# Optimization experiments

Hardware: AMD Instinct MI355X
Metric: run time of the kernel (lower is better)

Reference implementation:

```python
import jax, jax.numpy as jnp
import numpy as np

# Config constants (match init_kwargs)
D_MODEL = 1024
D_MLP = 2048
NUM_EXPERTS = 8
EXPERTS_PER_TOKEN = 2
BATCH, SEQ = 2, 2048


def setup_inputs() -> dict:
    key = jax.random.key(0)
    k0, k1, k2, k3, k4 = jax.random.split(key, 5)
    init = lambda k, shape: jax.random.normal(k, shape, jnp.float32) * 0.02
    return {
        "x": jax.random.normal(k0, (BATCH, SEQ, D_MODEL), jnp.float32),
        "W_router": init(k1, (D_MODEL, NUM_EXPERTS)),
        "W_gate": init(k2, (NUM_EXPERTS, D_MODEL, D_MLP)),
        "W_in": init(k3, (NUM_EXPERTS, D_MODEL, D_MLP)),
        "W_out": init(k4, (NUM_EXPERTS, D_MLP, D_MODEL)),
    }


def reference(x, W_router, W_gate, W_in, W_out):
    B, S, D = x.shape
    h = x.reshape(-1, D)                                  # [T, D]
    T = h.shape[0]
    E = W_router.shape[1]

    # Router: softmax in fp32, top-k, renormalize (as in torch source)
    router_logits = h @ W_router                          # [T, E]
    probs = jax.nn.softmax(router_logits.astype(jnp.float32), axis=-1)
    top_w, top_i = jax.lax.top_k(probs, EXPERTS_PER_TOKEN)  # [T, K]
    top_w = top_w / top_w.sum(axis=-1, keepdims=True)
    top_w = top_w.astype(h.dtype)

    # Dense combine matrix [T, E]; top-k indices are distinct per token
    combine = jnp.zeros((T, E), h.dtype).at[jnp.arange(T)[:, None], top_i].set(top_w)

    # GatedMLP per expert: silu(h @ Wg) * (h @ Wi) @ Wo  (computed densely over experts,
    # then combined with the sparse routing weights -> same math as gather/MLP/scatter loop)
    gate_pre = jnp.einsum('td,edf->etf', h, W_gate)       # [E, T, F]
    up = jnp.einsum('td,edf->etf', h, W_in)               # [E, T, F]
    act = jax.nn.silu(gate_pre) * up                      # [E, T, F]
    expert_out = jnp.einsum('etf,efd->etd', act, W_out)   # [E, T, D]

    out = jnp.einsum('etd,te->td', expert_out, combine)   # [T, D]
    return out.reshape(B, S, D), router_logits
```

## Files before the change

### kernel.cpp

```cpp
#include <hip/hip_runtime.h>
#include <cstdint>
#include <cstddef>

#define T_TOK 4096
#define DM 1024
#define DF 2048
#define NE 8
#define PADROWS 9216
#define MAXTILES 72

typedef unsigned short u16;
typedef unsigned int u32;
using short8 = __attribute__((ext_vector_type(8))) short;
using f32x4  = __attribute__((ext_vector_type(4))) float;

static constexpr size_t OFF_H    = 0;
static constexpr size_t OFF_WGT  = OFF_H   + (size_t)T_TOK * DM * 2;
static constexpr size_t OFF_WIT  = OFF_WGT + (size_t)NE * DM * DF * 2;
static constexpr size_t OFF_WOT  = OFF_WIT + (size_t)NE * DM * DF * 2;
static constexpr size_t OFF_A    = OFF_WOT + (size_t)NE * DF * DM * 2;
static constexpr size_t OFF_TOK  = OFF_A   + (size_t)PADROWS * DF * 2;
static constexpr size_t OFF_WL   = OFF_TOK + PADROWS * 4;
static constexpr size_t OFF_TEXP = OFF_WL  + PADROWS * 4;
static constexpr size_t OFF_TW   = OFF_TEXP + (size_t)T_TOK * 2 * 4;
static constexpr size_t OFF_CNT  = OFF_TW  + (size_t)T_TOK * 2 * 4;
static constexpr size_t OFF_CUR  = OFF_CNT + 64;
static constexpr size_t OFF_NT   = OFF_CUR + 64;
static constexpr size_t OFF_TE   = OFF_NT  + 64;
static constexpr size_t OFF_TP   = OFF_TE  + 512;
static constexpr size_t OFF_POS  = OFF_TP  + 512;

__device__ __forceinline__ u16 f2bf(float f) {
  u32 u = __builtin_bit_cast(u32, f);
  u += 0x7FFFu + ((u >> 16) & 1u);
  return (u16)(u >> 16);
}
__device__ __forceinline__ float bf2f(u16 b) {
  u32 u = ((u32)b) << 16;
  return __builtin_bit_cast(float, u);
}

__device__ __forceinline__ void async16(const void* g, void* l) {
  __builtin_amdgcn_global_load_lds((__attribute__((address_space(1))) void*)(g),
                                   (__attribute__((address_space(3))) void*)(l),
                                   16, 0, 0);
}

__global__ void init_small_k(int* __restrict__ tok, float* __restrict__ wl,
                             int* __restrict__ cnt) {
  int i = blockIdx.x * 256 + threadIdx.x;
  if (i < PADROWS) { tok[i] = -1; wl[i] = 0.f; }
  if (i < NE) cnt[i] = 0;
}

__global__ void transpose_w_k(const float* __restrict__ Wg, const float* __restrict__ Wi,
                              const float* __restrict__ Wo, u16* __restrict__ wgT,
                              u16* __restrict__ wiT, u16* __restrict__ woT) {
  __shared__ u16 lT[64][65];
  int bid = blockIdx.x;
  int mat = bid >> 12;
  int r = bid & 4095;
  const float* src; u16* dst; int R, C;
  if (mat == 0)      { src = Wg; dst = wgT; R = DM; C = DF; }
  else if (mat == 1) { src = Wi; dst = wiT; R = DM; C = DF; }
  else               { src = Wo; dst = woT; R = DF; C = DM; }
  int e = r >> 9;
  int rem = r & 511;
  int ctiles = C >> 6;
  int tr = rem / ctiles, tc = rem % ctiles;
  size_t eb = (size_t)e * R * C;
  int r0 = tr * 64, c0 = tc * 64;
  int wv = threadIdx.x >> 6, lane = threadIdx.x & 63;
#pragma unroll
  for (int it = 0; it < 16; ++it) {
    int rl = it * 4 + wv;
    float v = src[eb + (size_t)(r0 + rl) * C + c0 + lane];
    lT[lane][rl] = f2bf(v);
  }
  __syncthreads();
#pragma unroll
  for (int i = 0; i < 2; ++i) {
    const int cl = i * 32 + wv * 8 + (lane >> 3);
    const int b8 = (lane & 7) * 8;
    u16 tmp[8];
#pragma unroll
    for (int k = 0; k < 8; ++k) tmp[k] = lT[cl][b8 + k];
    *(short8*)&dst[eb + (size_t)(c0 + cl) * R + r0 + b8] = *(const short8*)tmp;
  }
}

__global__ void router_k(const float* __restrict__ x, const float* __restrict__ Wr,
                         float* __restrict__ logits, int* __restrict__ texp,
                         float* __restrict__ tw, int* __restrict__ cnt,
                         u16* __restrict__ hbf) {
  int wv = threadIdx.x >> 6, lane = threadIdx.x & 63;
  int t = blockIdx.x * 4 + wv;
  const float* h = x + (size_t)t * DM;
  u16* hb = hbf + (size_t)t * DM;
  float acc[8] = {0.f, 0.f, 0.f, 0.f, 0.f, 0.f, 0.f, 0.f};
#pragma unroll
  for (int j = 0; j < 16; ++j) {
    float hv = h[lane + j * 64];
    hb[lane + j * 64] = f2bf(hv);
    const float4* wr = (const float4*)(Wr + (size_t)(lane + j * 64) * 8);
    float4 w0 = wr[0], w1 = wr[1];
    acc[0] += hv * w0.x; acc[1] += hv * w0.y; acc[2] += hv * w0.z; acc[3] += hv * w0.w;
    acc[4] += hv * w1.x; acc[5] += hv * w1.y; acc[6] += hv * w1.z; acc[7] += hv * w1.w;
  }
#pragma unroll
  for (int e = 0; e < 8; ++e)
#pragma unroll
    for (int off = 32; off > 0; off >>= 1) acc[e] += __shfl_down(acc[e], off, 64);
  if (lane == 0) {
    float mx = acc[0];
#pragma unroll
    for (int e = 1; e < 8; ++e) mx = fmaxf(mx, acc[e]);
    float p[8];
#pragma unroll
    for (int e = 0; e < 8; ++e) p[e] = __expf(acc[e] - mx);
    int i1 = 0; float b1 = p[0];
#pragma unroll
    for (int e = 1; e < 8; ++e) if (p[e] > b1) { b1 = p[e]; i1 = e; }
    int i2 = -1; float b2 = -1.f;
#pragma unroll
    for (int e = 0; e < 8; ++e) if (e != i1 && p[e] > b2) { b2 = p[e]; i2 = e; }
    float inv = 1.f / (b1 + b2);
    texp[t * 2] = i1; texp[t * 2 + 1] = i2;
    tw[t * 2] = b1 * inv; tw[t * 2 + 1] = b2 * inv;
    atomicAdd(&cnt[i1], 1); atomicAdd(&cnt[i2], 1);
#pragma unroll
    for (int e = 0; e < 8; ++e) logits[(size_t)t * 8 + e] = acc[e];
  }
}

__global__ void plan_k(const int* __restrict__ cnt, int* __restrict__ cursor,
                       int* __restrict__ tile_e, int* __restrict__ tile_p,
                       int* __restrict__ ntiles) {
  __shared__ int toff[NE + 1], roff[NE];
  const int l = threadIdx.x;
  if (l == 0) {
    int o = 0, nt = 0;
    for (int e = 0; e < NE; ++e) {
      int t = (cnt[e] + 127) >> 7;
      cursor[e] = o; toff[e] = nt; roff[e] = o;
      nt += t; o += t * 128;
    }
    toff[NE] = nt;
    *ntiles = nt;
  }
  __syncthreads();
  for (int idx = l; idx < MAXTILES; idx += 64) {
    int e = 0;
    while (e < NE && !(idx >= toff[e] && idx < toff[e + 1])) ++e;
    if (e < NE) { tile_e[idx] = e; tile_p[idx] = roff[e] + (idx - toff[e]) * 128; }
  }
}

__global__ void scatter_k(const int* __restrict__ texp, const float* __restrict__ tw,
                          int* __restrict__ cursor, int* __restrict__ tok,
                          float* __restrict__ wl, int* __restrict__ pos) {
  int t = blockIdx.x * 256 + threadIdx.x;
#pragma unroll
  for (int k = 0; k < 2; ++k) {
    int e = texp[t * 2 + k];
    int p = atomicAdd(&cursor[e], 1);
    tok[p] = t;
    wl[p] = tw[t * 2 + k];
    pos[t * 2 + k] = p;
  }
}

__global__ __launch_bounds__(256) void gemm1_k(
    const u16* __restrict__ hbf, const u16* __restrict__ wgT, const u16* __restrict__ wiT,
    const int* __restrict__ tok, const float* __restrict__ wl,
    const int* __restrict__ tile_e, const int* __restrict__ tile_p,
    const int* __restrict__ ntiles, u16* __restrict__ Aact) {
  __shared__ char smem[65536];
  const int tile = blockIdx.y;
  if (tile >= *ntiles) return;
  const int e  = tile_e[tile];
  const int p0 = tile_p[tile];
  const int f0 = blockIdx.x * 64;
  const int tid = threadIdx.x, wv = tid >> 6, lane = tid & 63;

  const u16* hsrc[4];
  int hoff[4];
#pragma unroll
  for (int i = 0; i < 4; ++i) {
    const int row = wv * 32 + i * 8 + (lane >> 3);
    const int gc  = (lane & 7) ^ (row & 7);
    int tk  = tok[p0 + row];
    if (tk < 0) tk = 0;
    hsrc[i] = hbf + (size_t)tk * DM + gc * 8;
    hoff[i] = (wv * 32 + i * 8) * 64;
  }
  const u16* wbase = ((wv < 2) ? wgT : wiT) + (size_t)e * DM * DF;
  const int half = wv & 1, mt = wv >> 1;
  const u16* bsrc[4];
  int boff[4];
#pragma unroll
  for (int i = 0; i < 4; ++i) {
    const int row = half * 32 + i * 8 + (lane >> 3);
    const int gc  = (lane & 7) ^ (row & 7);
    bsrc[i] = wbase + (size_t)(f0 + row) * DM + gc * 8;
    boff[i] = 8192 + mt * 4096 + (half * 32 + i * 8) * 64;
  }

  f32x4 accG[4][2], accU[4][2];
#pragma unroll
  for (int m = 0; m < 4; ++m)
#pragma unroll
    for (int n = 0; n < 2; ++n) { accG[m][n] = (f32x4)(0.f); accU[m][n] = (f32x4)(0.f); }

  const int wr = wv >> 1, wc = wv & 1;
  const int wrBase = wr * 64, wcBase = wc * 32;
  const int l4 = lane >> 4, ln = lane & 15;

  {
    u16* b = (u16*)smem;
#pragma unroll
    for (int i = 0; i < 4; ++i) async16(hsrc[i], b + hoff[i]);
#pragma unroll
    for (int i = 0; i < 4; ++i) async16(bsrc[i], b + boff[i]);
  }
  __syncthreads();

  int cur = 0;
  for (int kt = 0; kt < DM / 64; ++kt) {
    if (kt < DM / 64 - 1) {
      u16* b = (u16*)smem + (cur ^ 1) * 16384;
#pragma unroll
      for (int i = 0; i < 4; ++i) async16(hsrc[i] + (size_t)(kt + 1) * 64, b + hoff[i]);
#pragma unroll
      for (int i = 0; i < 4; ++i) async16(bsrc[i] + (size_t)(kt + 1) * 64, b + boff[i]);
    }
    const u16* b = (const u16*)smem + cur * 16384;
#pragma unroll
    for (int s = 0; s < 2; ++s) {
      const int c = s * 4 + l4;
      short8 a[4], bg[2], bu[2];
#pragma unroll
      for (int m = 0; m < 4; ++m) {
        const int row = wrBase + m * 16 + ln;
        a[m] = *(const short8*)&b[row * 64 + ((c ^ (row & 7)) * 8)];
      }
#pragma unroll
      for (int n = 0; n < 2; ++n) {
        const int rowb = wcBase + n * 16 + ln;
        const int so = rowb * 64 + ((c ^ (rowb & 7)) * 8);
        bg[n] = *(const short8*)&b[8192 + so];
        bu[n] = *(const short8*)&b[12288 + so];
      }
#pragma unroll
      for (int m = 0; m < 4; ++m)
#pragma unroll
        for (int n = 0; n < 2; ++n) {
          accG[m][n] = __builtin_amdgcn_mfma_f32_16x16x32_bf16(a[m], bg[n], accG[m][n], 0, 0, 0);
          accU[m][n] = __builtin_amdgcn_mfma_f32_16x16x32_bf16(a[m], bu[n], accU[m][n], 0, 0, 0);
        }
    }
    __syncthreads();
    cur ^= 1;
  }

  u16* lOut = (u16*)smem;
#pragma unroll
  for (int m = 0; m < 4; ++m)
#pragma unroll
    for (int j = 0; j < 4; ++j) {
      const int row = wrBase + m * 16 + l4 * 4 + j;
      const float w = wl[p0 + row];
#pragma unroll
      for (int n = 0; n < 2; ++n) {
        const float g = accG[m][n][j];
        const float u = accU[m][n][j];
        const float val = (g / (1.f + __expf(-g))) * u * w;
        lOut[row * 80 + wcBase + n * 16 + ln] = f2bf(val);
      }
    }
  __syncthreads();
  const int r = tid >> 1, hf = tid & 1;
  u16* gdst = Aact + (size_t)(p0 + r) * DF + f0 + hf * 32;
  const u16* lsrc = &lOut[r * 80 + hf * 32];
#pragma unroll
  for (int i = 0; i < 4; ++i)
    *(short8*)(gdst + i * 8) = *(const short8*)(lsrc + i * 8);
}

__global__ __launch_bounds__(256) void gemm2_k(
    const u16* __restrict__ Aact, const u16* __restrict__ woT,
    const int* __restrict__ tile_e, const int* __restrict__ tile_p,
    const int* __restrict__ ntiles, u16* __restrict__ scr) {
  __shared__ char smem[49152];
  const int tile = blockIdx.y;
  if (tile >= *ntiles) return;
  const int e  = tile_e[tile];
  const int p0 = tile_p[tile];
  const int d0 = blockIdx.x * 64;
  const int tid = threadIdx.x, wv = tid >> 6, lane = tid & 63;

  const u16* asrc[4];
  int aoff[4];
#pragma unroll
  for (int i = 0; i < 4; ++i) {
    const int row = wv * 32 + i * 8 + (lane >> 3);
    const int gc  = (lane & 7) ^ (row & 7);
    asrc[i] = Aact + (size_t)(p0 + row) * DF + gc * 8;
    aoff[i] = (wv * 32 + i * 8) * 64;
  }
  const u16* wb = woT + (size_t)e * DM * DF;
  const u16* wsrc[2];
  int woff[2];
#pragma unroll
  for (int i = 0; i < 2; ++i) {
    const int row = wv * 16 + i * 8 + (lane >> 3);
    const int gc  = (lane & 7) ^ (row & 7);
    wsrc[i] = wb + (size_t)(d0 + row) * DF + gc * 8;
    woff[i] = 8192 + (wv * 16 + i * 8) * 64;
  }

  f32x4 acc[4][2];
#pragma unroll
  for (int m = 0; m < 4; ++m)
#pragma unroll
    for (int n = 0; n < 2; ++n) acc[m][n] = (f32x4)(0.f);

  const int wr = wv >> 1, wc = wv & 1;
  const int wrBase = wr * 64, wcBase = wc * 32;
  const int l4 = lane >> 4, ln = lane & 15;

  {
    u16* b = (u16*)smem;
#pragma unroll
    for (int i = 0; i < 4; ++i) async16(asrc[i], b + aoff[i]);
#pragma unroll
    for (int i = 0; i < 2; ++i) async16(wsrc[i], b + woff[i]);
  }
  __syncthreads();

  int cur = 0;
  for (int kt = 0; kt < DF / 64; ++kt) {
    if (kt < DF / 64 - 1) {
      u16* b = (u16*)smem + (cur ^ 1) * 12288;
#pragma unroll
      for (int i = 0; i < 4; ++i) async16(asrc[i] + (size_t)(kt + 1) * 64, b + aoff[i]);
#pragma unroll
      for (int i = 0; i < 2; ++i) async16(wsrc[i] + (size_t)(kt + 1) * 64, b + woff[i]);
    }
    const u16* b = (const u16*)smem + cur * 12288;
#pragma unroll
    for (int s = 0; s < 2; ++s) {
      const int c = s * 4 + l4;
      short8 a[4], bw[2];
#pragma unroll
      for (int m = 0; m < 4; ++m) {
        const int row = wrBase + m * 16 + ln;
        a[m] = *(const short8*)&b[row * 64 + ((c ^ (row & 7)) * 8)];
      }
#pragma unroll
      for (int n = 0; n < 2; ++n) {
        const int rowb = wcBase + n * 16 + ln;
        bw[n] = *(const short8*)&b[8192 + rowb * 64 + ((c ^ (rowb & 7)) * 8)];
      }
#pragma unroll
      for (int m = 0; m < 4; ++m)
#pragma unroll
        for (int n = 0; n < 2; ++n)
          acc[m][n] = __builtin_amdgcn_mfma_f32_16x16x32_bf16(a[m], bw[n], acc[m][n], 0, 0, 0);
    }
    __syncthreads();
    cur ^= 1;
  }

  u16* lOut = (u16*)smem;
#pragma unroll
  for (int m = 0; m < 4; ++m)
#pragma unroll
    for (int j = 0; j < 4; ++j) {
      const int row = wrBase + m * 16 + l4 * 4 + j;
#pragma unroll
      for (int n = 0; n < 2; ++n)
        lOut[row * 72 + wcBase + n * 16 + ln] = f2bf(acc[m][n][j]);
    }
  __syncthreads();
  const int r = tid >> 1, hf = tid & 1;
  u16* gdst = scr + (size_t)(p0 + r) * DM + d0 + hf * 32;
  const u16* lsrc = &lOut[r * 72 + hf * 32];
#pragma unroll
  for (int i = 0; i < 4; ++i)
    *(short8*)(gdst + i * 8) = *(const short8*)(lsrc + i * 8);
}

__global__ void combine_k(const u16* __restrict__ scr, const int* __restrict__ pos,
                          float* __restrict__ out) {
  const int t = blockIdx.x;
  const int d = threadIdx.x;
  const int p1 = pos[t * 2], p2 = pos[t * 2 + 1];
  const ushort4 a = *(const ushort4*)(scr + (size_t)p1 * DM + d * 4);
  const ushort4 b = *(const ushort4*)(scr + (size_t)p2 * DM + d * 4);
  float4 o;
  o.x = bf2f(a.x) + bf2f(b.x);
  o.y = bf2f(a.y) + bf2f(b.y);
  o.z = bf2f(a.z) + bf2f(b.z);
  o.w = bf2f(a.w) + bf2f(b.w);
  *(float4*)(out + (size_t)t * DM + d * 4) = o;
}

extern "C" void kernel_launch(void* const* d_in, const int* in_sizes, int n_in,
                              void* d_out, int out_size, void* d_ws, size_t ws_size,
                              hipStream_t stream) {
  const float* x  = (const float*)d_in[0];
  const float* Wr = (const float*)d_in[1];
  const float* Wg = (const float*)d_in[2];
  const float* Wi = (const float*)d_in[3];
  const float* Wo = (const float*)d_in[4];
  float* outF = (float*)d_out;
  float* logits = outF + (size_t)T_TOK * DM;

  char* ws = (char*)d_ws;
  u16*  hbf   = (u16*)(ws + OFF_H);
  u16*  wgT   = (u16*)(ws + OFF_WGT);
  u16*  wiT   = (u16*)(ws + OFF_WIT);
  u16*  woT   = (u16*)(ws + OFF_WOT);
  u16*  Aact  = (u16*)(ws + OFF_A);
  int*  tok   = (int*)(ws + OFF_TOK);
  float* wl   = (float*)(ws + OFF_WL);
  int*  texp  = (int*)(ws + OFF_TEXP);
  float* tw   = (float*)(ws + OFF_TW);
  int*  cnt   = (int*)(ws + OFF_CNT);
  int*  cur   = (int*)(ws + OFF_CUR);
  int*  nt    = (int*)(ws + OFF_NT);
  int*  te    = (int*)(ws + OFF_TE);
  int*  tp    = (int*)(ws + OFF_TP);
  int*  pos   = (int*)(ws + OFF_POS);
  u16*  scr   = (u16*)(ws + OFF_WGT);

  init_small_k<<<40, 256, 0, stream>>>(tok, wl, cnt);
  transpose_w_k<<<12288, 256, 0, stream>>>(Wg, Wi, Wo, wgT, wiT, woT);
  router_k<<<1024, 256, 0, stream>>>(x, Wr, logits, texp, tw, cnt, hbf);
  plan_k<<<1, 64, 0, stream>>>(cnt, cur, te, tp, nt);
  scatter_k<<<16, 256, 0, stream>>>(texp, tw, cur, tok, wl, pos);
  gemm1_k<<<dim3(DF / 64, MAXTILES), 256, 0, stream>>>(hbf, wgT, wiT, tok, wl, te, tp, nt, Aact);
  gemm2_k<<<dim3(DM / 64, MAXTILES), 256, 0, stream>>>(Aact, woT, te, tp, nt, scr);
  combine_k<<<4096, 256, 0, stream>>>(scr, pos, outF);
}
```

Measured before the change: 347.1 us.

## Load GEMM weight operands directly to registers with 4-stage LDS pipeline for activations

Both expert GEMMs now read the B (weight) fragments straight from global memory into registers, double-buffered, instead of staging them through LDS. The activation tile goes through a 4-slot LDS ring with manual vmcnt waits and a single barrier per k-step, and MFMA blocks are wrapped in s_setprio. Separately, the plan and scatter kernels are merged into one single-block kernel that uses LDS atomics for the cursors. The aim is to cut LDS traffic and barrier stalls and deepen prefetch, at the cost of uncoalesced per-lane global weight loads, higher register pressure, and a serialized scatter running in one block.

```diff
diff --git a/kernel.cpp b/kernel.cpp
--- a/kernel.cpp
+++ b/kernel.cpp
@@ -45,6 +45,9 @@
                                    (__attribute__((address_space(3))) void*)(l),
                                    16, 0, 0);
 }
+
+#define VMW(N) asm volatile("s_waitcnt vmcnt(" #N ")" ::: "memory")
+#define BAR() __builtin_amdgcn_s_barrier()
 
 __global__ void init_small_k(int* __restrict__ tok, float* __restrict__ wl,
                              int* __restrict__ cnt) {
@@ -133,40 +136,38 @@
   }
 }
 
-__global__ void plan_k(const int* __restrict__ cnt, int* __restrict__ cursor,
-                       int* __restrict__ tile_e, int* __restrict__ tile_p,
-                       int* __restrict__ ntiles) {
+__global__ void plan_scatter_k(const int* __restrict__ cnt, const int* __restrict__ texp,
+                               const float* __restrict__ tw, int* __restrict__ tile_e,
+                               int* __restrict__ tile_p, int* __restrict__ ntiles,
+                               int* __restrict__ tok, float* __restrict__ wl,
+                               int* __restrict__ pos) {
+  __shared__ int curs[NE];
   __shared__ int toff[NE + 1], roff[NE];
-  const int l = threadIdx.x;
-  if (l == 0) {
-    int o = 0, nt = 0;
+  if (threadIdx.x == 0) {
+    int off = 0, nt = 0;
     for (int e = 0; e < NE; ++e) {
-      int t = (cnt[e] + 127) >> 7;
-      cursor[e] = o; toff[e] = nt; roff[e] = o;
-      nt += t; o += t * 128;
+      int tt = (cnt[e] + 127) >> 7;
+      curs[e] = off; toff[e] = nt; roff[e] = off;
+      nt += tt; off += tt * 128;
     }
     toff[NE] = nt;
     *ntiles = nt;
   }
   __syncthreads();
-  for (int idx = l; idx < MAXTILES; idx += 64) {
+  for (int idx = threadIdx.x; idx < MAXTILES; idx += 256) {
     int e = 0;
     while (e < NE && !(idx >= toff[e] && idx < toff[e + 1])) ++e;
     if (e < NE) { tile_e[idx] = e; tile_p[idx] = roff[e] + (idx - toff[e]) * 128; }
   }
-}
-
-__global__ void scatter_k(const int* __restrict__ texp, const float* __restrict__ tw,
-                          int* __restrict__ cursor, int* __restrict__ tok,
-                          float* __restrict__ wl, int* __restrict__ pos) {
-  int t = blockIdx.x * 256 + threadIdx.x;
-#pragma unroll
-  for (int k = 0; k < 2; ++k) {
-    int e = texp[t * 2 + k];
-    int p = atomicAdd(&cursor[e], 1);
-    tok[p] = t;
-    wl[p] = tw[t * 2 + k];
-    pos[t * 2 + k] = p;
+  for (int t = threadIdx.x; t < T_TOK; t += 256) {
+#pragma unroll
+    for (int k = 0; k < 2; ++k) {
+      int e = texp[t * 2 + k];
+      int p = atomicAdd(&curs[e], 1);
+      tok[p] = t;
+      wl[p] = tw[t * 2 + k];
+      pos[t * 2 + k] = p;
+    }
   }
 }
 
@@ -175,7 +176,7 @@
     const int* __restrict__ tok, const float* __restrict__ wl,
     const int* __restrict__ tile_e, const int* __restrict__ tile_p,
     const int* __restrict__ ntiles, u16* __restrict__ Aact) {
-  __shared__ char smem[65536];
+  __shared__ u16 smem[4 * 8192];
   const int tile = blockIdx.y;
   if (tile >= *ntiles) return;
   const int e  = tile_e[tile];
@@ -194,76 +195,87 @@
     hsrc[i] = hbf + (size_t)tk * DM + gc * 8;
     hoff[i] = (wv * 32 + i * 8) * 64;
   }
-  const u16* wbase = ((wv < 2) ? wgT : wiT) + (size_t)e * DM * DF;
-  const int half = wv & 1, mt = wv >> 1;
-  const u16* bsrc[4];
-  int boff[4];
-#pragma unroll
-  for (int i = 0; i < 4; ++i) {
-    const int row = half * 32 + i * 8 + (lane >> 3);
-    const int gc  = (lane & 7) ^ (row & 7);
-    bsrc[i] = wbase + (size_t)(f0 + row) * DM + gc * 8;
-    boff[i] = 8192 + mt * 4096 + (half * 32 + i * 8) * 64;
-  }
-
-  f32x4 accG[4][2], accU[4][2];
-#pragma unroll
-  for (int m = 0; m < 4; ++m)
-#pragma unroll
-    for (int n = 0; n < 2; ++n) { accG[m][n] = (f32x4)(0.f); accU[m][n] = (f32x4)(0.f); }
 
   const int wr = wv >> 1, wc = wv & 1;
   const int wrBase = wr * 64, wcBase = wc * 32;
   const int l4 = lane >> 4, ln = lane & 15;
 
-  {
-    u16* b = (u16*)smem;
-#pragma unroll
-    for (int i = 0; i < 4; ++i) async16(hsrc[i], b + hoff[i]);
-#pragma unroll
-    for (int i = 0; i < 4; ++i) async16(bsrc[i], b + boff[i]);
-  }
-  __syncthreads();
-
-  int cur = 0;
-  for (int kt = 0; kt < DM / 64; ++kt) {
-    if (kt < DM / 64 - 1) {
-      u16* b = (u16*)smem + (cur ^ 1) * 16384;
-#pragma unroll
-      for (int i = 0; i < 4; ++i) async16(hsrc[i] + (size_t)(kt + 1) * 64, b + hoff[i]);
-#pragma unroll
-      for (int i = 0; i < 4; ++i) async16(bsrc[i] + (size_t)(kt + 1) * 64, b + boff[i]);
-    }
-    const u16* b = (const u16*)smem + cur * 16384;
+  const u16* bgb[2];
+  const u16* bub[2];
+#pragma unroll
+  for (int n = 0; n < 2; ++n) {
+    const size_t rowf = (size_t)(f0 + wcBase + n * 16 + ln);
+    bgb[n] = wgT + (size_t)e * DM * DF + rowf * DM + l4 * 8;
+    bub[n] = wiT + (size_t)e * DM * DF + rowf * DM + l4 * 8;
+  }
+
+  f32x4 accG[4][2], accU[4][2];
+#pragma unroll
+  for (int m = 0; m < 4; ++m)
+#pragma unroll
+    for (int n = 0; n < 2; ++n) { accG[m][n] = (f32x4)(0.f); accU[m][n] = (f32x4)(0.f); }
+
+  short8 bg0[2][2], bu0[2][2], bg1[2][2], bu1[2][2];
+
+  auto stageH = [&](int T) {
+    u16* dst = smem + (T & 3) * 8192;
+#pragma unroll
+    for (int i = 0; i < 4; ++i) async16(hsrc[i] + (size_t)T * 64, dst + hoff[i]);
+  };
+  auto loadB = [&](short8 (&bg)[2][2], short8 (&bu)[2][2], int T) {
+#pragma unroll
+    for (int n = 0; n < 2; ++n)
+#pragma unroll
+      for (int s = 0; s < 2; ++s) {
+        bg[n][s] = *(const short8*)(bgb[n] + (size_t)T * 64 + s * 32);
+        bu[n][s] = *(const short8*)(bub[n] + (size_t)T * 64 + s * 32);
+      }
+  };
+  auto comp = [&](const short8 (&bg)[2][2], const short8 (&bu)[2][2], int slot) {
+    const u16* b = smem + slot * 8192;
+    short8 a[4][2];
 #pragma unroll
     for (int s = 0; s < 2; ++s) {
       const int c = s * 4 + l4;
-      short8 a[4], bg[2], bu[2];
 #pragma unroll
       for (int m = 0; m < 4; ++m) {
         const int row = wrBase + m * 16 + ln;
-        a[m] = *(const short8*)&b[row * 64 + ((c ^ (row & 7)) * 8)];
+        a[m][s] = *(const short8*)&b[row * 64 + ((c ^ (row & 7)) * 8)];
       }
-#pragma unroll
-      for (int n = 0; n < 2; ++n) {
-        const int rowb = wcBase + n * 16 + ln;
-        const int so = rowb * 64 + ((c ^ (rowb & 7)) * 8);
-        bg[n] = *(const short8*)&b[8192 + so];
-        bu[n] = *(const short8*)&b[12288 + so];
-      }
+    }
+    __builtin_amdgcn_s_setprio(1);
+#pragma unroll
+    for (int s = 0; s < 2; ++s)
 #pragma unroll
       for (int m = 0; m < 4; ++m)
 #pragma unroll
         for (int n = 0; n < 2; ++n) {
-          accG[m][n] = __builtin_amdgcn_mfma_f32_16x16x32_bf16(a[m], bg[n], accG[m][n], 0, 0, 0);
-          accU[m][n] = __builtin_amdgcn_mfma_f32_16x16x32_bf16(a[m], bu[n], accU[m][n], 0, 0, 0);
+          accG[m][n] = __builtin_amdgcn_mfma_f32_16x16x32_bf16(a[m][s], bg[n][s], accG[m][n], 0, 0, 0);
+          accU[m][n] = __builtin_amdgcn_mfma_f32_16x16x32_bf16(a[m][s], bu[n][s], accU[m][n], 0, 0, 0);
         }
-    }
-    __syncthreads();
-    cur ^= 1;
-  }
-
-  u16* lOut = (u16*)smem;
+    __builtin_amdgcn_s_setprio(0);
+  };
+
+  stageH(0);
+  loadB(bg0, bu0, 0);
+  stageH(1);
+  VMW(4); BAR();
+
+  for (int t = 0; t < 14; t += 2) {
+    loadB(bg1, bu1, t + 1); stageH(t + 2);
+    comp(bg0, bu0, t & 3);
+    VMW(12); BAR();
+    loadB(bg0, bu0, t + 2); stageH(t + 3);
+    comp(bg1, bu1, (t + 1) & 3);
+    VMW(12); BAR();
+  }
+  loadB(bg1, bu1, 15);
+  comp(bg0, bu0, 2);
+  VMW(8); BAR();
+  comp(bg1, bu1, 3);
+
+  u16* lOut = smem;
+  BAR();
 #pragma unroll
   for (int m = 0; m < 4; ++m)
 #pragma unroll
@@ -291,7 +303,7 @@
     const u16* __restrict__ Aact, const u16* __restrict__ woT,
     const int* __restrict__ tile_e, const int* __restrict__ tile_p,
     const int* __restrict__ ntiles, u16* __restrict__ scr) {
-  __shared__ char smem[49152];
+  __shared__ u16 smem[4 * 8192];
   const int tile = blockIdx.y;
   if (tile >= *ntiles) return;
   const int e  = tile_e[tile];
@@ -308,71 +320,81 @@
     asrc[i] = Aact + (size_t)(p0 + row) * DF + gc * 8;
     aoff[i] = (wv * 32 + i * 8) * 64;
   }
-  const u16* wb = woT + (size_t)e * DM * DF;
-  const u16* wsrc[2];
-  int woff[2];
-#pragma unroll
-  for (int i = 0; i < 2; ++i) {
-    const int row = wv * 16 + i * 8 + (lane >> 3);
-    const int gc  = (lane & 7) ^ (row & 7);
-    wsrc[i] = wb + (size_t)(d0 + row) * DF + gc * 8;
-    woff[i] = 8192 + (wv * 16 + i * 8) * 64;
-  }
-
-  f32x4 acc[4][2];
-#pragma unroll
-  for (int m = 0; m < 4; ++m)
-#pragma unroll
-    for (int n = 0; n < 2; ++n) acc[m][n] = (f32x4)(0.f);
 
   const int wr = wv >> 1, wc = wv & 1;
   const int wrBase = wr * 64, wcBase = wc * 32;
   const int l4 = lane >> 4, ln = lane & 15;
 
-  {
-    u16* b = (u16*)smem;
-#pragma unroll
-    for (int i = 0; i < 4; ++i) async16(asrc[i], b + aoff[i]);
-#pragma unroll
-    for (int i = 0; i < 2; ++i) async16(wsrc[i], b + woff[i]);
-  }
-  __syncthreads();
-
-  int cur = 0;
-  for (int kt = 0; kt < DF / 64; ++kt) {
-    if (kt < DF / 64 - 1) {
-      u16* b = (u16*)smem + (cur ^ 1) * 12288;
-#pragma unroll
-      for (int i = 0; i < 4; ++i) async16(asrc[i] + (size_t)(kt + 1) * 64, b + aoff[i]);
-#pragma unroll
-      for (int i = 0; i < 2; ++i) async16(wsrc[i] + (size_t)(kt + 1) * 64, b + woff[i]);
-    }
-    const u16* b = (const u16*)smem + cur * 12288;
+  const u16* bwb[2];
+#pragma unroll
+  for (int n = 0; n < 2; ++n) {
+    const size_t rowd = (size_t)(d0 + wcBase + n * 16 + ln);
+    bwb[n] = woT + (size_t)e * DM * DF + rowd * DF + l4 * 8;
+  }
+
+  f32x4 acc[4][2];
+#pragma unroll
+  for (int m = 0; m < 4; ++m)
+#pragma unroll
+    for (int n = 0; n < 2; ++n) acc[m][n] = (f32x4)(0.f);
+
+  short8 bw0[2][2], bw1[2][2];
+
+  auto stageA = [&](int T) {
+    u16* dst = smem + (T & 3) * 8192;
+#pragma unroll
+    for (int i = 0; i < 4; ++i) async16(asrc[i] + (size_t)T * 64, dst + aoff[i]);
+  };
+  auto loadB = [&](short8 (&bw)[2][2], int T) {
+#pragma unroll
+    for (int n = 0; n < 2; ++n)
+#pragma unroll
+      for (int s = 0; s < 2; ++s)
+        bw[n][s] = *(const short8*)(bwb[n] + (size_t)T * 64 + s * 32);
+  };
+  auto comp = [&](const short8 (&bw)[2][2], int slot) {
+    const u16* b = smem + slot * 8192;
+    short8 a[4][2];
 #pragma unroll
     for (int s = 0; s < 2; ++s) {
       const int c = s * 4 + l4;
-      short8 a[4], bw[2];
 #pragma unroll
       for (int m = 0; m < 4; ++m) {
         const int row = wrBase + m * 16 + ln;
-        a[m] = *(const short8*)&b[row * 64 + ((c ^ (row & 7)) * 8)];
+        a[m][s] = *(const short8*)&b[row * 64 + ((c ^ (row & 7)) * 8)];
       }
-#pragma unroll
-      for (int n = 0; n < 2; ++n) {
-        const int rowb = wcBase + n * 16 + ln;
-        bw[n] = *(const short8*)&b[8192 + rowb * 64 + ((c ^ (rowb & 7)) * 8)];
-      }
+    }
+    __builtin_amdgcn_s_setprio(1);
+#pragma unroll
+    for (int s = 0; s < 2; ++s)
 #pragma unroll
       for (int m = 0; m < 4; ++m)
 #pragma unroll
         for (int n = 0; n < 2; ++n)
-          acc[m][n] = __builtin_amdgcn_mfma_f32_16x16x32_bf16(a[m], bw[n], acc[m][n], 0, 0, 0);
-    }
-    __syncthreads();
-    cur ^= 1;
-  }
-
-  u16* lOut = (u16*)smem;
+          acc[m][n] = __builtin_amdgcn_mfma_f32_16x16x32_bf16(a[m][s], bw[n][s], acc[m][n], 0, 0, 0);
+    __builtin_amdgcn_s_setprio(0);
+  };
+
+  stageA(0);
+  loadB(bw0, 0);
+  stageA(1);
+  VMW(4); BAR();
+
+  for (int t = 0; t < 30; t += 2) {
+    loadB(bw1, t + 1); stageA(t + 2);
+    comp(bw0, t & 3);
+    VMW(8); BAR();
+    loadB(bw0, t + 2); stageA(t + 3);
+    comp(bw1, (t + 1) & 3);
+    VMW(8); BAR();
+  }
+  loadB(bw1, 31);
+  comp(bw0, 2);
+  VMW(4); BAR();
+  comp(bw1, 3);
+
+  u16* lOut = smem;
+  BAR();
 #pragma unroll
   for (int m = 0; m < 4; ++m)
 #pragma unroll
@@ -428,7 +450,6 @@
   int*  texp  = (int*)(ws + OFF_TEXP);
   float* tw   = (float*)(ws + OFF_TW);
   int*  cnt   = (int*)(ws + OFF_CNT);
-  int*  cur   = (int*)(ws + OFF_CUR);
   int*  nt    = (int*)(ws + OFF_NT);
   int*  te    = (int*)(ws + OFF_TE);
   int*  tp    = (int*)(ws + OFF_TP);
@@ -438,8 +459,7 @@
   init_small_k<<<40, 256, 0, stream>>>(tok, wl, cnt);
   transpose_w_k<<<12288, 256, 0, stream>>>(Wg, Wi, Wo, wgT, wiT, woT);
   router_k<<<1024, 256, 0, stream>>>(x, Wr, logits, texp, tw, cnt, hbf);
-  plan_k<<<1, 64, 0, stream>>>(cnt, cur, te, tp, nt);
-  scatter_k<<<16, 256, 0, stream>>>(texp, tw, cur, tok, wl, pos);
+  plan_scatter_k<<<1, 256, 0, stream>>>(cnt, texp, tw, te, tp, nt, tok, wl, pos);
   gemm1_k<<<dim3(DF / 64, MAXTILES), 256, 0, stream>>>(hbf, wgT, wiT, tok, wl, te, tp, nt, Aact);
   gemm2_k<<<dim3(DM / 64, MAXTILES), 256, 0, stream>>>(Aact, woT, te, tp, nt, scr);
   combine_k<<<4096, 256, 0, stream>>>(scr, pos, outF);
```

After: 494.1 us. 1.42x slower.
